# Optimization experiments

Measured on AMD Instinct MI355X. Metric: run time of the kernel, lower is better.

## Reference

```python
import jax, jax.numpy as jnp
import numpy as np

DIM = 1024
HIDDEN = 2048
NUM_EXPERTS = 8
TOP_K = 2


def setup_inputs() -> dict:
    key = jax.random.key(0)
    ks = jax.random.split(key, 6)
    scale = 0.02
    x = jax.random.normal(ks[0], (2, 4096, DIM), dtype=jnp.float32)
    # router: Linear(dim, num_experts, bias=False) -> weight [E, d]
    router_w = jax.random.normal(ks[1], (NUM_EXPERTS, DIM), dtype=jnp.float32) * scale
    # per-expert MLP: Linear(d, h) -> w1 [E, h, d], b1 [E, h]; Linear(h, d) -> w2 [E, d, h], b2 [E, d]
    w1 = jax.random.normal(ks[2], (NUM_EXPERTS, HIDDEN, DIM), dtype=jnp.float32) * scale
    b1 = jnp.zeros((NUM_EXPERTS, HIDDEN), dtype=jnp.float32)
    w2 = jax.random.normal(ks[3], (NUM_EXPERTS, DIM, HIDDEN), dtype=jnp.float32) * scale
    b2 = jnp.zeros((NUM_EXPERTS, DIM), dtype=jnp.float32)
    return {"x": x, "router_w": router_w, "w1": w1, "b1": b1, "w2": w2, "b2": b2}


def reference(x, router_w, w1, b1, w2, b2):
    b, s, d = x.shape
    xf = x.reshape(-1, d)                              # [T, d]
    logits = xf @ router_w.T                           # [T, E]
    all_probs = jax.nn.softmax(logits, axis=-1)
    topk_logits, topk_inds = jax.lax.top_k(logits, TOP_K)   # [T, K]
    topk_probs = jax.nn.softmax(topk_logits, axis=-1)
    E = router_w.shape[0]
    onehot = jax.nn.one_hot(topk_inds, E, dtype=xf.dtype)   # [T, K, E]
    # combine weights per (token, expert); zero where expert not selected
    gate = jnp.einsum('tke,tk->te', onehot, topk_probs)     # [T, E]
    # load-balancing auxiliary loss
    f_i = onehot.mean(axis=(0, 1))                          # [E]
    P_i = all_probs.mean(axis=0)                            # [E]
    aux_loss = E * jnp.sum(f_i * P_i)
    # dense per-expert MLP, weighted combine (dropout=0 / eval mode)
    out = jnp.zeros_like(xf)
    for e in range(E):  # fixed small loop over experts
        h = jax.nn.gelu(xf @ w1[e].T + b1[e], approximate=False)  # exact GELU (torch default)
        y = h @ w2[e].T + b2[e]
        out = out + gate[:, e:e + 1] * y
    return out.reshape(b, s, d), aux_loss
```

## Files before the change

### kernel.cpp

```cpp
#include <hip/hip_runtime.h>


#define TOKS 8192
#define DIMD 1024
#define HID  2048
#define NE   8

#define OFF_COUNTS   0
#define OFF_OFFSETS  64
#define OFF_CURSORS  128
#define OFF_TILEOFF  192
#define OFF_TOPKI    256
#define OFF_TOPKG    (OFF_TOPKI + TOKS*2*4)
#define OFF_BLKPS    (OFF_TOPKG + TOKS*2*4)
#define OFF_ATOK     (OFF_BLKPS + 2048*NE*4)
#define OFF_AGATE    (OFF_ATOK + TOKS*2*4)
#define OFF_PINV     (OFF_AGATE + TOKS*2*4)
#define OFF_XG       (1u << 20)
#define XG_ROWS      (TOKS*2 + 128)
#define OFF_W1B      (OFF_XG  + (size_t)XG_ROWS * DIMD * 2)
#define OFF_W2B      (OFF_W1B + (size_t)NE * HID * DIMD * 2)
#define OFF_H        (OFF_W2B + (size_t)NE * DIMD * HID * 2)
#define OFF_Y        (OFF_H   + (size_t)XG_ROWS * HID * 2)

typedef __bf16 bf16x8 __attribute__((ext_vector_type(8)));
typedef float  floatx4 __attribute__((ext_vector_type(4)));

__device__ __forceinline__ float bf2f(unsigned short u) {
    return __uint_as_float(((unsigned)u) << 16);
}
__device__ __forceinline__ unsigned short f2bf(float f) {
    unsigned u = __float_as_uint(f);
    unsigned r = (u + 0x7FFFu + ((u >> 16) & 1u)) >> 16;
    return (unsigned short)r;
}

#define GLOBAL_AS(p) ((const __attribute__((address_space(1))) unsigned int*)(p))
#define LDS_AS(p)    ((__attribute__((address_space(3))) unsigned int*)(p))

__global__ __launch_bounds__(256) void head_kernel(
    const float* __restrict__ x, const float* __restrict__ rw,
    int* __restrict__ topki, float* __restrict__ topkg,
    float* __restrict__ blkps,
    const float4* __restrict__ w1, ushort4* __restrict__ w1b, int n1,
    const float4* __restrict__ w2, ushort4* __restrict__ w2b, int n2)
{
    if (blockIdx.x >= 2048) {
        int i = (blockIdx.x - 2048) * 256 + threadIdx.x;
        int stride = 8192 * 256;
        int ntot = n1 + n2;
        for (; i < ntot; i += stride) {
            float4 v; ushort4 o;
            if (i < n1) v = w1[i]; else v = w2[i - n1];
            o.x = f2bf(v.x); o.y = f2bf(v.y); o.z = f2bf(v.z); o.w = f2bf(v.w);
            if (i < n1) w1b[i] = o; else w2b[i - n1] = o;
        }
        return;
    }

    int wave = threadIdx.x >> 6;
    int lane = threadIdx.x & 63;
    int t = blockIdx.x * 4 + wave;
    const float* xt = x + (size_t)t * DIMD;

    float acc[NE];
#pragma unroll
    for (int e = 0; e < NE; e++) acc[e] = 0.f;
    for (int i = 0; i < DIMD / 64; i++) {
        float xv = xt[lane + 64 * i];
#pragma unroll
        for (int e = 0; e < NE; e++) acc[e] += xv * rw[e * DIMD + lane + 64 * i];
    }
#pragma unroll
    for (int off = 32; off > 0; off >>= 1) {
#pragma unroll
        for (int e = 0; e < NE; e++) acc[e] += __shfl_down(acc[e], off);
    }

    __shared__ float ps[4][NE];
    if (lane == 0) {
        float m = acc[0];
#pragma unroll
        for (int e = 1; e < NE; e++) m = fmaxf(m, acc[e]);
        float ex[NE], s = 0.f;
#pragma unroll
        for (int e = 0; e < NE; e++) { ex[e] = expf(acc[e] - m); s += ex[e]; }
        float inv = 1.f / s;
#pragma unroll
        for (int e = 0; e < NE; e++) ps[wave][e] = ex[e] * inv;

        int i0 = 0; float l0 = acc[0];
#pragma unroll
        for (int e = 1; e < NE; e++) if (acc[e] > l0) { l0 = acc[e]; i0 = e; }
        int i1 = -1; float l1 = -3.4e38f;
#pragma unroll
        for (int e = 0; e < NE; e++) if (e != i0 && acc[e] > l1) { l1 = acc[e]; i1 = e; }
        float e1 = expf(l1 - l0);
        float g0 = 1.f / (1.f + e1);
        float g1 = e1 * g0;
        topki[t * 2 + 0] = i0; topki[t * 2 + 1] = i1;
        topkg[t * 2 + 0] = g0; topkg[t * 2 + 1] = g1;
    }
    __syncthreads();
    if (threadIdx.x < NE) {
        float s = ps[0][threadIdx.x] + ps[1][threadIdx.x] + ps[2][threadIdx.x] + ps[3][threadIdx.x];
        blkps[blockIdx.x * NE + threadIdx.x] = s;
    }
}

__global__ __launch_bounds__(256) void finalize_kernel(
    const int* __restrict__ topki, const float* __restrict__ blkps,
    int* __restrict__ counts, int* __restrict__ offsets, int* __restrict__ cursors,
    int* __restrict__ tileoff, float* __restrict__ aux_out)
{
    __shared__ float psum[NE];
    __shared__ int cnt[NE];
    int tid = threadIdx.x;
    if (tid < NE) { psum[tid] = 0.f; cnt[tid] = 0; }
    __syncthreads();

    float lp[NE]; int lc[NE];
#pragma unroll
    for (int e = 0; e < NE; e++) { lp[e] = 0.f; lc[e] = 0; }
    const float4* bp4 = (const float4*)blkps;
    for (int i = tid; i < 2048 * NE / 4; i += 256) {
        float4 v = bp4[i];
        int eb = (4 * i) & 7;
        lp[eb + 0] += v.x; lp[eb + 1] += v.y; lp[eb + 2] += v.z; lp[eb + 3] += v.w;
    }
    const int4* ti4 = (const int4*)topki;
    for (int i = tid; i < TOKS * 2 / 4; i += 256) {
        int4 v = ti4[i];
        lc[v.x]++; lc[v.y]++; lc[v.z]++; lc[v.w]++;
    }
#pragma unroll
    for (int e = 0; e < NE; e++) { atomicAdd(&psum[e], lp[e]); atomicAdd(&cnt[e], lc[e]); }
    __syncthreads();

    if (tid == 0) {
        int off = 0, to = 0;
        for (int e = 0; e < NE; e++) {
            counts[e] = cnt[e];
            offsets[e] = off; cursors[e] = off;
            tileoff[e] = to;
            off += cnt[e];
            to += (cnt[e] + 127) >> 7;
        }
        offsets[NE] = off; tileoff[NE] = to;
        float aux = 0.f;
        for (int e = 0; e < NE; e++)
            aux += ((float)cnt[e] / (float)(TOKS * 2)) * (psum[e] / (float)TOKS);
        aux_out[0] = (float)NE * aux;
    }
}

__global__ __launch_bounds__(64) void fill_kernel(
    const int* __restrict__ topki, const float* __restrict__ topkg,
    int* __restrict__ cursors, int* __restrict__ atok, float* __restrict__ agate,
    int* __restrict__ posinv)
{
    int lane = threadIdx.x;
    int t = blockIdx.x * 64 + lane;
    unsigned long long below = (lane == 63) ? 0x7FFFFFFFFFFFFFFFull
                                            : ((1ull << lane) - 1ull);
#pragma unroll
    for (int k = 0; k < 2; k++) {
        int e = topki[t * 2 + k];
        float g = topkg[t * 2 + k];
        for (int ee = 0; ee < NE; ee++) {
            bool pred = (e == ee);
            unsigned long long mask = __ballot(pred ? 1 : 0);
            if (mask) {
                int leader = __ffsll((unsigned long long)mask) - 1;
                int base = 0;
                if (lane == leader) base = atomicAdd(&cursors[ee], (int)__popcll(mask));
                base = __shfl(base, leader);
                if (pred) {
                    int pos = base + (int)__popcll(mask & below);
                    atok[pos] = t;
                    agate[pos] = g;
                    posinv[t * 2 + k] = pos;
                }
            }
        }
    }
}

__global__ __launch_bounds__(256) void gather_x_kernel(
    const float* __restrict__ x, const int* __restrict__ atok,
    ushort* __restrict__ Xg)
{
    int r = blockIdx.x;
    int tid = threadIdx.x;
    int tok = atok[r];
    float4 v = ((const float4*)(x + (size_t)tok * DIMD))[tid];
    ushort4 o;
    o.x = f2bf(v.x); o.y = f2bf(v.y); o.z = f2bf(v.z); o.w = f2bf(v.w);
    ((ushort4*)(Xg + (size_t)r * DIMD))[tid] = o;
}

__global__ __launch_bounds__(256) void phase1_kernel(
    const ushort* __restrict__ Xg, const ushort* __restrict__ w1b,
    const float* __restrict__ b1,
    const int* __restrict__ counts, const int* __restrict__ offsets,
    const int* __restrict__ tileoff, unsigned short* __restrict__ Hbuf)
{
    const int NCOLT = HID / 128;
    int total = tileoff[NE] * NCOLT;
    int chunk = gridDim.x >> 3;
    int idx = (blockIdx.x & 7) * chunk + (blockIdx.x >> 3);
    if (idx >= total) return;
    int ct = idx & (NCOLT - 1);
    int rowt = idx / NCOLT;
    int e = 0;
    while (rowt >= tileoff[e + 1]) e++;
    int row0 = (rowt - tileoff[e]) * 128;
    int cnt = counts[e];
    int base = offsets[e];
    int colbase = ct * 128;

    __shared__ ushort ldsA[128 * 32];
    __shared__ ushort ldsB[128 * 32];

    int tid = threadIdx.x;
    int lane = tid & 63;
    int wave = tid >> 6;
    int wrow = wave >> 1, wcol = wave & 1;
    int l15 = lane & 15, quad = lane >> 4;

    const ushort* gA0 = Xg + (size_t)(base + row0 + 16 * (2 * wave)     + l15) * DIMD + quad * 8;
    const ushort* gA1 = Xg + (size_t)(base + row0 + 16 * (2 * wave + 1) + l15) * DIMD + quad * 8;
    const ushort* wB  = w1b + (size_t)e * HID * DIMD;
    const ushort* gB0 = wB + (size_t)(colbase + 16 * (2 * wave)     + l15) * DIMD + quad * 8;
    const ushort* gB1 = wB + (size_t)(colbase + 16 * (2 * wave + 1) + l15) * DIMD + quad * 8;

    ushort* ldA0 = &ldsA[(2 * wave) * 512];
    ushort* ldA1 = &ldsA[(2 * wave + 1) * 512];
    ushort* ldB0 = &ldsB[(2 * wave) * 512];
    ushort* ldB1 = &ldsB[(2 * wave + 1) * 512];

    floatx4 acc[4][4];
#pragma unroll
    for (int i = 0; i < 4; i++)
#pragma unroll
        for (int j = 0; j < 4; j++) acc[i][j] = (floatx4){0.f, 0.f, 0.f, 0.f};

    const bf16x8* fA = reinterpret_cast<const bf16x8*>(ldsA);
    const bf16x8* fB = reinterpret_cast<const bf16x8*>(ldsB);

    for (int k0 = 0; k0 < DIMD; k0 += 32) {
        __syncthreads();
        __builtin_amdgcn_global_load_lds(GLOBAL_AS(gA0), LDS_AS(ldA0), 16, 0, 0);
        __builtin_amdgcn_global_load_lds(GLOBAL_AS(gA1), LDS_AS(ldA1), 16, 0, 0);
        __builtin_amdgcn_global_load_lds(GLOBAL_AS(gB0), LDS_AS(ldB0), 16, 0, 0);
        __builtin_amdgcn_global_load_lds(GLOBAL_AS(gB1), LDS_AS(ldB1), 16, 0, 0);
        gA0 += 32; gA1 += 32; gB0 += 32; gB1 += 32;
        __syncthreads();

        bf16x8 a[4], b[4];
#pragma unroll
        for (int i = 0; i < 4; i++) a[i] = fA[(4 * wrow + i) * 64 + lane];
#pragma unroll
        for (int j = 0; j < 4; j++) b[j] = fB[(4 * wcol + j) * 64 + lane];
#pragma unroll
        for (int i = 0; i < 4; i++)
#pragma unroll
            for (int j = 0; j < 4; j++)
                acc[i][j] = __builtin_amdgcn_mfma_f32_16x16x32_bf16(a[i], b[j], acc[i][j], 0, 0, 0);
    }

#pragma unroll
    for (int i = 0; i < 4; i++) {
#pragma unroll
        for (int r = 0; r < 4; r++) {
            int pr = row0 + 64 * wrow + 16 * i + quad * 4 + r;
            if (pr < cnt) {
                size_t hrow = (size_t)(base + pr) * HID;
#pragma unroll
                for (int j = 0; j < 4; j++) {
                    int col = colbase + 64 * wcol + 16 * j + l15;
                    float v = acc[i][j][r] + b1[e * HID + col];
                    v = 0.5f * v * (1.f + erff(v * 0.70710678118654752f));
                    Hbuf[hrow + col] = f2bf(v);
                }
            }
        }
    }
}

__global__ __launch_bounds__(256) void phase2_kernel(
    const ushort* __restrict__ Hbuf, const ushort* __restrict__ w2b,
    const int* __restrict__ counts, const int* __restrict__ offsets,
    const int* __restrict__ tileoff, ushort* __restrict__ Y)
{
    const int NCOLT = DIMD / 128;
    int total = tileoff[NE] * NCOLT;
    int chunk = gridDim.x >> 3;
    int idx = (blockIdx.x & 7) * chunk + (blockIdx.x >> 3);
    if (idx >= total) return;
    int ct = idx & (NCOLT - 1);
    int rowt = idx / NCOLT;
    int e = 0;
    while (rowt >= tileoff[e + 1]) e++;
    int row0 = (rowt - tileoff[e]) * 128;
    int cnt = counts[e];
    int base = offsets[e];
    int colbase = ct * 128;

    __shared__ ushort ldsA[128 * 32];
    __shared__ ushort ldsB[128 * 32];

    int tid = threadIdx.x;
    int lane = tid & 63;
    int wave = tid >> 6;
    int wrow = wave >> 1, wcol = wave & 1;
    int l15 = lane & 15, quad = lane >> 4;

    const ushort* gA0 = Hbuf + (size_t)(base + row0 + 16 * (2 * wave)     + l15) * HID + quad * 8;
    const ushort* gA1 = Hbuf + (size_t)(base + row0 + 16 * (2 * wave + 1) + l15) * HID + quad * 8;
    const ushort* wB  = w2b + (size_t)e * DIMD * HID;
    const ushort* gB0 = wB + (size_t)(colbase + 16 * (2 * wave)     + l15) * HID + quad * 8;
    const ushort* gB1 = wB + (size_t)(colbase + 16 * (2 * wave + 1) + l15) * HID + quad * 8;

    ushort* ldA0 = &ldsA[(2 * wave) * 512];
    ushort* ldA1 = &ldsA[(2 * wave + 1) * 512];
    ushort* ldB0 = &ldsB[(2 * wave) * 512];
    ushort* ldB1 = &ldsB[(2 * wave + 1) * 512];

    floatx4 acc[4][4];
#pragma unroll
    for (int i = 0; i < 4; i++)
#pragma unroll
        for (int j = 0; j < 4; j++) acc[i][j] = (floatx4){0.f, 0.f, 0.f, 0.f};

    const bf16x8* fA = reinterpret_cast<const bf16x8*>(ldsA);
    const bf16x8* fB = reinterpret_cast<const bf16x8*>(ldsB);

    for (int k0 = 0; k0 < HID; k0 += 32) {
        __syncthreads();
        __builtin_amdgcn_global_load_lds(GLOBAL_AS(gA0), LDS_AS(ldA0), 16, 0, 0);
        __builtin_amdgcn_global_load_lds(GLOBAL_AS(gA1), LDS_AS(ldA1), 16, 0, 0);
        __builtin_amdgcn_global_load_lds(GLOBAL_AS(gB0), LDS_AS(ldB0), 16, 0, 0);
        __builtin_amdgcn_global_load_lds(GLOBAL_AS(gB1), LDS_AS(ldB1), 16, 0, 0);
        gA0 += 32; gA1 += 32; gB0 += 32; gB1 += 32;
        __syncthreads();

        bf16x8 a[4], b[4];
#pragma unroll
        for (int i = 0; i < 4; i++) a[i] = fA[(4 * wrow + i) * 64 + lane];
#pragma unroll
        for (int j = 0; j < 4; j++) b[j] = fB[(4 * wcol + j) * 64 + lane];
#pragma unroll
        for (int i = 0; i < 4; i++)
#pragma unroll
            for (int j = 0; j < 4; j++)
                acc[i][j] = __builtin_amdgcn_mfma_f32_16x16x32_bf16(a[i], b[j], acc[i][j], 0, 0, 0);
    }

#pragma unroll
    for (int i = 0; i < 4; i++) {
#pragma unroll
        for (int r = 0; r < 4; r++) {
            int pr = row0 + 64 * wrow + 16 * i + quad * 4 + r;
            if (pr < cnt) {
                size_t yrow = (size_t)(base + pr) * DIMD;
#pragma unroll
                for (int j = 0; j < 4; j++) {
                    int col = colbase + 64 * wcol + 16 * j + l15;
                    Y[yrow + col] = f2bf(acc[i][j][r]);
                }
            }
        }
    }
}

__global__ __launch_bounds__(256) void combine_kernel(
    const ushort* __restrict__ Y, const float* __restrict__ b2,
    const int* __restrict__ topki, const float* __restrict__ topkg,
    const int* __restrict__ posinv, float* __restrict__ out)
{
    int wave = threadIdx.x >> 6;
    int lane = threadIdx.x & 63;
    int t = blockIdx.x * 4 + wave;
    int e0 = topki[t * 2 + 0], e1 = topki[t * 2 + 1];
    float g0 = topkg[t * 2 + 0], g1 = topkg[t * 2 + 1];
    int p0 = posinv[t * 2 + 0], p1 = posinv[t * 2 + 1];

    const ushort4* y0 = (const ushort4*)(Y + (size_t)p0 * DIMD);
    const ushort4* y1 = (const ushort4*)(Y + (size_t)p1 * DIMD);
    const float4* b20 = (const float4*)(b2 + (size_t)e0 * DIMD);
    const float4* b21 = (const float4*)(b2 + (size_t)e1 * DIMD);
    float4* o4 = (float4*)(out + (size_t)t * DIMD);

#pragma unroll
    for (int c = 0; c < DIMD / 4 / 64; c++) {
        int i = lane + 64 * c;
        ushort4 a = y0[i], b = y1[i];
        float4 ba = b20[i], bb = b21[i];
        float4 r;
        r.x = g0 * (bf2f(a.x) + ba.x) + g1 * (bf2f(b.x) + bb.x);
        r.y = g0 * (bf2f(a.y) + ba.y) + g1 * (bf2f(b.y) + bb.y);
        r.z = g0 * (bf2f(a.z) + ba.z) + g1 * (bf2f(b.z) + bb.z);
        r.w = g0 * (bf2f(a.w) + ba.w) + g1 * (bf2f(b.w) + bb.w);
        o4[i] = r;
    }
}

extern "C" void kernel_launch(void* const* d_in, const int* in_sizes, int n_in,
                              void* d_out, int out_size, void* d_ws, size_t ws_size,
                              hipStream_t stream) {
    const float* x  = (const float*)d_in[0];
    const float* rw = (const float*)d_in[1];
    const float* w1 = (const float*)d_in[2];
    const float* b1 = (const float*)d_in[3];
    const float* w2 = (const float*)d_in[4];
    const float* b2 = (const float*)d_in[5];
    float* out = (float*)d_out;

    char* ws = (char*)d_ws;
    int*   counts  = (int*)(ws + OFF_COUNTS);
    int*   offsets = (int*)(ws + OFF_OFFSETS);
    int*   cursors = (int*)(ws + OFF_CURSORS);
    int*   tileoff = (int*)(ws + OFF_TILEOFF);
    int*   topki   = (int*)(ws + OFF_TOPKI);
    float* topkg   = (float*)(ws + OFF_TOPKG);
    float* blkps   = (float*)(ws + OFF_BLKPS);
    int*   atok    = (int*)(ws + OFF_ATOK);
    float* agate   = (float*)(ws + OFF_AGATE);
    int*   posinv  = (int*)(ws + OFF_PINV);
    ushort* Xg     = (ushort*)(ws + OFF_XG);
    ushort* w1b    = (ushort*)(ws + OFF_W1B);
    ushort* w2b    = (ushort*)(ws + OFF_W2B);
    ushort* Hbuf   = (ushort*)(ws + OFF_H);
    ushort* Y      = (ushort*)(ws + OFF_Y);

    head_kernel<<<10240, 256, 0, stream>>>(
        x, rw, topki, topkg, blkps,
        (const float4*)w1, (ushort4*)w1b, NE * HID * DIMD / 4,
        (const float4*)w2, (ushort4*)w2b, NE * DIMD * HID / 4);

    finalize_kernel<<<1, 256, 0, stream>>>(topki, blkps, counts, offsets, cursors,
                                           tileoff, out + (size_t)TOKS * DIMD);
    fill_kernel<<<TOKS / 64, 64, 0, stream>>>(topki, topkg, cursors, atok, agate,
                                              posinv);
    gather_x_kernel<<<TOKS * 2, 256, 0, stream>>>(x, atok, Xg);

    phase1_kernel<<<135 * (HID / 128), 256, 0, stream>>>(
        Xg, w1b, b1, counts, offsets, tileoff, Hbuf);
    phase2_kernel<<<135 * (DIMD / 128), 256, 0, stream>>>(
        Hbuf, w2b, counts, offsets, tileoff, Y);
    combine_kernel<<<TOKS / 4, 256, 0, stream>>>(Y, b2, topki, topkg, posinv, out);
}
```

Before: 642.6 us.

## Fuse token gather and weight conversion into the expert GEMM loads

Phase 1 now reads fp32 token rows directly through the routing index and converts them to bf16 while staging into LDS. That removes the separate gather kernel and the Xg buffer. Phase 2 converts fp32 w2 on the fly instead of relying on a pre-converted w2b copy, which shrinks the head kernel's conversion work. The finalize and fill kernels are merged into a single-block kernel that uses LDS cursors. In exchange, A/B tiles go through registers rather than async global-to-LDS loads, fp32 data is re-read once per tile, and the scatter now runs serially in one block.

```diff
diff --git a/kernel.cpp b/kernel.cpp
--- a/kernel.cpp
+++ b/kernel.cpp
@@ -14,8 +14,7 @@
 #define OFF_TOPKG    (OFF_TOPKI + TOKS*2*4)
 #define OFF_BLKPS    (OFF_TOPKG + TOKS*2*4)
 #define OFF_ATOK     (OFF_BLKPS + 2048*NE*4)
-#define OFF_AGATE    (OFF_ATOK + TOKS*2*4)
-#define OFF_PINV     (OFF_AGATE + TOKS*2*4)
+#define OFF_PINV     (OFF_ATOK + TOKS*2*4 + TOKS*2*4)
 #define OFF_XG       (1u << 20)
 #define XG_ROWS      (TOKS*2 + 128)
 #define OFF_W1B      (OFF_XG  + (size_t)XG_ROWS * DIMD * 2)
@@ -25,6 +24,7 @@
 
 typedef __bf16 bf16x8 __attribute__((ext_vector_type(8)));
 typedef float  floatx4 __attribute__((ext_vector_type(4)));
+typedef unsigned short ushortx8 __attribute__((ext_vector_type(8)));
 
 __device__ __forceinline__ float bf2f(unsigned short u) {
     return __uint_as_float(((unsigned)u) << 16);
@@ -34,6 +34,12 @@
     unsigned r = (u + 0x7FFFu + ((u >> 16) & 1u)) >> 16;
     return (unsigned short)r;
 }
+__device__ __forceinline__ ushortx8 cvt8(float4 a, float4 b) {
+    ushortx8 r;
+    r[0] = f2bf(a.x); r[1] = f2bf(a.y); r[2] = f2bf(a.z); r[3] = f2bf(a.w);
+    r[4] = f2bf(b.x); r[5] = f2bf(b.y); r[6] = f2bf(b.z); r[7] = f2bf(b.w);
+    return r;
+}
 
 #define GLOBAL_AS(p) ((const __attribute__((address_space(1))) unsigned int*)(p))
 #define LDS_AS(p)    ((__attribute__((address_space(3))) unsigned int*)(p))
@@ -42,18 +48,16 @@
     const float* __restrict__ x, const float* __restrict__ rw,
     int* __restrict__ topki, float* __restrict__ topkg,
     float* __restrict__ blkps,
-    const float4* __restrict__ w1, ushort4* __restrict__ w1b, int n1,
-    const float4* __restrict__ w2, ushort4* __restrict__ w2b, int n2)
+    const float4* __restrict__ w1, ushort4* __restrict__ w1b, int n1)
 {
     if (blockIdx.x >= 2048) {
         int i = (blockIdx.x - 2048) * 256 + threadIdx.x;
-        int stride = 8192 * 256;
-        int ntot = n1 + n2;
-        for (; i < ntot; i += stride) {
-            float4 v; ushort4 o;
-            if (i < n1) v = w1[i]; else v = w2[i - n1];
+        int stride = 4096 * 256;
+        for (; i < n1; i += stride) {
+            float4 v = w1[i];
+            ushort4 o;
             o.x = f2bf(v.x); o.y = f2bf(v.y); o.z = f2bf(v.z); o.w = f2bf(v.w);
-            if (i < n1) w1b[i] = o; else w2b[i - n1] = o;
+            w1b[i] = o;
         }
         return;
     }
@@ -108,13 +112,16 @@
     }
 }
 
-__global__ __launch_bounds__(256) void finalize_kernel(
-    const int* __restrict__ topki, const float* __restrict__ blkps,
-    int* __restrict__ counts, int* __restrict__ offsets, int* __restrict__ cursors,
-    int* __restrict__ tileoff, float* __restrict__ aux_out)
+__global__ __launch_bounds__(256) void finfill_kernel(
+    const int* __restrict__ topki, const float* __restrict__ topkg,
+    const float* __restrict__ blkps,
+    int* __restrict__ counts, int* __restrict__ offsets,
+    int* __restrict__ tileoff, float* __restrict__ aux_out,
+    int* __restrict__ atok, int* __restrict__ posinv)
 {
     __shared__ float psum[NE];
     __shared__ int cnt[NE];
+    __shared__ int curs[NE];
     int tid = threadIdx.x;
     if (tid < NE) { psum[tid] = 0.f; cnt[tid] = 0; }
     __syncthreads();
@@ -141,7 +148,8 @@
         int off = 0, to = 0;
         for (int e = 0; e < NE; e++) {
             counts[e] = cnt[e];
-            offsets[e] = off; cursors[e] = off;
+            offsets[e] = off;
+            curs[e] = off;
             tileoff[e] = to;
             off += cnt[e];
             to += (cnt[e] + 127) >> 7;
@@ -152,58 +160,36 @@
             aux += ((float)cnt[e] / (float)(TOKS * 2)) * (psum[e] / (float)TOKS);
         aux_out[0] = (float)NE * aux;
     }
-}
-
-__global__ __launch_bounds__(64) void fill_kernel(
-    const int* __restrict__ topki, const float* __restrict__ topkg,
-    int* __restrict__ cursors, int* __restrict__ atok, float* __restrict__ agate,
-    int* __restrict__ posinv)
-{
-    int lane = threadIdx.x;
-    int t = blockIdx.x * 64 + lane;
-    unsigned long long below = (lane == 63) ? 0x7FFFFFFFFFFFFFFFull
-                                            : ((1ull << lane) - 1ull);
-#pragma unroll
-    for (int k = 0; k < 2; k++) {
-        int e = topki[t * 2 + k];
-        float g = topkg[t * 2 + k];
+    __syncthreads();
+
+    int lane = tid & 63;
+    unsigned long long below = (1ull << lane) - 1ull;
+    for (int i = tid; i < TOKS * 2; i += 256) {
+        int e = topki[i];
         for (int ee = 0; ee < NE; ee++) {
             bool pred = (e == ee);
             unsigned long long mask = __ballot(pred ? 1 : 0);
             if (mask) {
                 int leader = __ffsll((unsigned long long)mask) - 1;
                 int base = 0;
-                if (lane == leader) base = atomicAdd(&cursors[ee], (int)__popcll(mask));
+                if (lane == leader) base = atomicAdd(&curs[ee], (int)__popcll(mask));
                 base = __shfl(base, leader);
                 if (pred) {
                     int pos = base + (int)__popcll(mask & below);
-                    atok[pos] = t;
-                    agate[pos] = g;
-                    posinv[t * 2 + k] = pos;
+                    atok[pos] = i >> 1;
+                    posinv[i] = pos;
                 }
             }
         }
     }
 }
 
-__global__ __launch_bounds__(256) void gather_x_kernel(
-    const float* __restrict__ x, const int* __restrict__ atok,
-    ushort* __restrict__ Xg)
-{
-    int r = blockIdx.x;
-    int tid = threadIdx.x;
-    int tok = atok[r];
-    float4 v = ((const float4*)(x + (size_t)tok * DIMD))[tid];
-    ushort4 o;
-    o.x = f2bf(v.x); o.y = f2bf(v.y); o.z = f2bf(v.z); o.w = f2bf(v.w);
-    ((ushort4*)(Xg + (size_t)r * DIMD))[tid] = o;
-}
-
 __global__ __launch_bounds__(256) void phase1_kernel(
-    const ushort* __restrict__ Xg, const ushort* __restrict__ w1b,
+    const float* __restrict__ x, const ushort* __restrict__ w1b,
     const float* __restrict__ b1,
     const int* __restrict__ counts, const int* __restrict__ offsets,
-    const int* __restrict__ tileoff, unsigned short* __restrict__ Hbuf)
+    const int* __restrict__ tileoff, const int* __restrict__ atok,
+    unsigned short* __restrict__ Hbuf)
 {
     const int NCOLT = HID / 128;
     int total = tileoff[NE] * NCOLT;
@@ -228,14 +214,18 @@
     int wrow = wave >> 1, wcol = wave & 1;
     int l15 = lane & 15, quad = lane >> 4;
 
-    const ushort* gA0 = Xg + (size_t)(base + row0 + 16 * (2 * wave)     + l15) * DIMD + quad * 8;
-    const ushort* gA1 = Xg + (size_t)(base + row0 + 16 * (2 * wave + 1) + l15) * DIMD + quad * 8;
+    int r0 = row0 + 16 * (2 * wave)     + l15;
+    int r1 = row0 + 16 * (2 * wave + 1) + l15;
+    int tok0 = (r0 < cnt) ? atok[base + r0] : 0;
+    int tok1 = (r1 < cnt) ? atok[base + r1] : 0;
+    const float* xr0 = x + (size_t)tok0 * DIMD + quad * 8;
+    const float* xr1 = x + (size_t)tok1 * DIMD + quad * 8;
+    ushortx8* wA0 = (ushortx8*)&ldsA[(2 * wave) * 512 + lane * 8];
+    ushortx8* wA1 = (ushortx8*)&ldsA[(2 * wave + 1) * 512 + lane * 8];
+
     const ushort* wB  = w1b + (size_t)e * HID * DIMD;
     const ushort* gB0 = wB + (size_t)(colbase + 16 * (2 * wave)     + l15) * DIMD + quad * 8;
     const ushort* gB1 = wB + (size_t)(colbase + 16 * (2 * wave + 1) + l15) * DIMD + quad * 8;
-
-    ushort* ldA0 = &ldsA[(2 * wave) * 512];
-    ushort* ldA1 = &ldsA[(2 * wave + 1) * 512];
     ushort* ldB0 = &ldsB[(2 * wave) * 512];
     ushort* ldB1 = &ldsB[(2 * wave + 1) * 512];
 
@@ -249,12 +239,16 @@
     const bf16x8* fB = reinterpret_cast<const bf16x8*>(ldsB);
 
     for (int k0 = 0; k0 < DIMD; k0 += 32) {
+        float4 a00 = *(const float4*)(xr0 + k0);
+        float4 a01 = *(const float4*)(xr0 + k0 + 4);
+        float4 a10 = *(const float4*)(xr1 + k0);
+        float4 a11 = *(const float4*)(xr1 + k0 + 4);
         __syncthreads();
-        __builtin_amdgcn_global_load_lds(GLOBAL_AS(gA0), LDS_AS(ldA0), 16, 0, 0);
-        __builtin_amdgcn_global_load_lds(GLOBAL_AS(gA1), LDS_AS(ldA1), 16, 0, 0);
         __builtin_amdgcn_global_load_lds(GLOBAL_AS(gB0), LDS_AS(ldB0), 16, 0, 0);
         __builtin_amdgcn_global_load_lds(GLOBAL_AS(gB1), LDS_AS(ldB1), 16, 0, 0);
-        gA0 += 32; gA1 += 32; gB0 += 32; gB1 += 32;
+        gB0 += 32; gB1 += 32;
+        *wA0 = cvt8(a00, a01);
+        *wA1 = cvt8(a10, a11);
         __syncthreads();
 
         bf16x8 a[4], b[4];
@@ -289,7 +283,7 @@
 }
 
 __global__ __launch_bounds__(256) void phase2_kernel(
-    const ushort* __restrict__ Hbuf, const ushort* __restrict__ w2b,
+    const ushort* __restrict__ Hbuf, const float* __restrict__ w2,
     const int* __restrict__ counts, const int* __restrict__ offsets,
     const int* __restrict__ tileoff, ushort* __restrict__ Y)
 {
@@ -318,14 +312,14 @@
 
     const ushort* gA0 = Hbuf + (size_t)(base + row0 + 16 * (2 * wave)     + l15) * HID + quad * 8;
     const ushort* gA1 = Hbuf + (size_t)(base + row0 + 16 * (2 * wave + 1) + l15) * HID + quad * 8;
-    const ushort* wB  = w2b + (size_t)e * DIMD * HID;
-    const ushort* gB0 = wB + (size_t)(colbase + 16 * (2 * wave)     + l15) * HID + quad * 8;
-    const ushort* gB1 = wB + (size_t)(colbase + 16 * (2 * wave + 1) + l15) * HID + quad * 8;
-
     ushort* ldA0 = &ldsA[(2 * wave) * 512];
     ushort* ldA1 = &ldsA[(2 * wave + 1) * 512];
-    ushort* ldB0 = &ldsB[(2 * wave) * 512];
-    ushort* ldB1 = &ldsB[(2 * wave + 1) * 512];
+
+    const float* wB = w2 + (size_t)e * DIMD * HID;
+    const float* wr0 = wB + (size_t)(colbase + 16 * (2 * wave)     + l15) * HID + quad * 8;
+    const float* wr1 = wB + (size_t)(colbase + 16 * (2 * wave + 1) + l15) * HID + quad * 8;
+    ushortx8* wBw0 = (ushortx8*)&ldsB[(2 * wave) * 512 + lane * 8];
+    ushortx8* wBw1 = (ushortx8*)&ldsB[(2 * wave + 1) * 512 + lane * 8];
 
     floatx4 acc[4][4];
 #pragma unroll
@@ -337,12 +331,16 @@
     const bf16x8* fB = reinterpret_cast<const bf16x8*>(ldsB);
 
     for (int k0 = 0; k0 < HID; k0 += 32) {
+        float4 b00 = *(const float4*)(wr0 + k0);
+        float4 b01 = *(const float4*)(wr0 + k0 + 4);
+        float4 b10 = *(const float4*)(wr1 + k0);
+        float4 b11 = *(const float4*)(wr1 + k0 + 4);
         __syncthreads();
         __builtin_amdgcn_global_load_lds(GLOBAL_AS(gA0), LDS_AS(ldA0), 16, 0, 0);
         __builtin_amdgcn_global_load_lds(GLOBAL_AS(gA1), LDS_AS(ldA1), 16, 0, 0);
-        __builtin_amdgcn_global_load_lds(GLOBAL_AS(gB0), LDS_AS(ldB0), 16, 0, 0);
-        __builtin_amdgcn_global_load_lds(GLOBAL_AS(gB1), LDS_AS(ldB1), 16, 0, 0);
-        gA0 += 32; gA1 += 32; gB0 += 32; gB1 += 32;
+        gA0 += 32; gA1 += 32;
+        *wBw0 = cvt8(b00, b01);
+        *wBw1 = cvt8(b10, b11);
         __syncthreads();
 
         bf16x8 a[4], b[4];
@@ -420,34 +418,27 @@
     char* ws = (char*)d_ws;
     int*   counts  = (int*)(ws + OFF_COUNTS);
     int*   offsets = (int*)(ws + OFF_OFFSETS);
-    int*   cursors = (int*)(ws + OFF_CURSORS);
     int*   tileoff = (int*)(ws + OFF_TILEOFF);
     int*   topki   = (int*)(ws + OFF_TOPKI);
     float* topkg   = (float*)(ws + OFF_TOPKG);
     float* blkps   = (float*)(ws + OFF_BLKPS);
     int*   atok    = (int*)(ws + OFF_ATOK);
-    float* agate   = (float*)(ws + OFF_AGATE);
     int*   posinv  = (int*)(ws + OFF_PINV);
-    ushort* Xg     = (ushort*)(ws + OFF_XG);
     ushort* w1b    = (ushort*)(ws + OFF_W1B);
-    ushort* w2b    = (ushort*)(ws + OFF_W2B);
     ushort* Hbuf   = (ushort*)(ws + OFF_H);
     ushort* Y      = (ushort*)(ws + OFF_Y);
 
-    head_kernel<<<10240, 256, 0, stream>>>(
+    head_kernel<<<6144, 256, 0, stream>>>(
         x, rw, topki, topkg, blkps,
-        (const float4*)w1, (ushort4*)w1b, NE * HID * DIMD / 4,
-        (const float4*)w2, (ushort4*)w2b, NE * DIMD * HID / 4);
-
-    finalize_kernel<<<1, 256, 0, stream>>>(topki, blkps, counts, offsets, cursors,
-                                           tileoff, out + (size_t)TOKS * DIMD);
-    fill_kernel<<<TOKS / 64, 64, 0, stream>>>(topki, topkg, cursors, atok, agate,
-                                              posinv);
-    gather_x_kernel<<<TOKS * 2, 256, 0, stream>>>(x, atok, Xg);
+        (const float4*)w1, (ushort4*)w1b, NE * HID * DIMD / 4);
+
+    finfill_kernel<<<1, 256, 0, stream>>>(topki, topkg, blkps, counts, offsets,
+                                          tileoff, out + (size_t)TOKS * DIMD,
+                                          atok, posinv);
 
     phase1_kernel<<<135 * (HID / 128), 256, 0, stream>>>(
-        Xg, w1b, b1, counts, offsets, tileoff, Hbuf);
+        x, w1b, b1, counts, offsets, tileoff, atok, Hbuf);
     phase2_kernel<<<135 * (DIMD / 128), 256, 0, stream>>>(
-        Hbuf, w2b, counts, offsets, tileoff, Y);
+        Hbuf, w2, counts, offsets, tileoff, Y);
     combine_kernel<<<TOKS / 4, 256, 0, stream>>>(Y, b2, topki, topkg, posinv, out);
 }
```

Result: slower. 792.0 us (+23.2%).
